# Performance work log

Hardware: AMD Instinct MI355X
Metric: run time of the kernel (lower is better)

The kernel has to match this reference:

```python
import jax, jax.numpy as jnp
import numpy as np

N, K, CIN, COUT, HF, WF = 8, 8, 128, 128, 64, 64
HT, WT = 128, 128
WIN_H = 20


def cos_window(size, h):
    t = np.linspace(0.0, np.pi / 2, h)
    s = np.sin(t)
    win = np.ones(size, dtype=np.float64)
    win[:h, :] = s[:, None]
    win[-h:, :] = s[::-1][:, None]
    win[:, :h] = s[None, :]
    win[:, -h:] = s[::-1][None, :]
    t2 = np.pi / 2 - np.sqrt(t[:, None] ** 2 + t[None, :] ** 2)
    s2 = np.sin(np.clip(t2, 0.0, None))
    win[:h, :h] = s2[::-1, ::-1]
    win[:h, -h:] = s2[::-1, :]
    win[-h:, :h] = s2[:, ::-1]
    win[-h:, -h:] = s2
    return win.astype(np.float32)


def setup_inputs() -> dict:
    key = jax.random.key(0)
    k1, k2, k3, k4 = jax.random.split(key, 4)
    x = jax.random.normal(k1, (N * K, CIN, HF, WF), dtype=jnp.float32)
    conv_w = jax.random.normal(k2, (COUT, CIN), dtype=jnp.float32) / np.sqrt(CIN).astype(np.float32)
    conv_b = jax.random.normal(k3, (COUT,), dtype=jnp.float32) * 0.1
    qs = jax.random.uniform(k4, (N, K, 2), dtype=jnp.float32, minval=0.5, maxval=1.5)
    rng = np.random.default_rng(0)
    bx = rng.integers(-8, 48, (N, K))
    by = rng.integers(-8, 48, (N, K))
    bw = rng.integers(32, 112, (N, K))
    bh = rng.integers(32, 112, (N, K))
    boxes = jnp.asarray(np.stack([bx, by, bx + bw, by + bh], axis=-1).astype(np.int32))
    win = jnp.asarray(cos_window((HT, WT), WIN_H))
    return {"x": x, "conv_w": conv_w, "conv_b": conv_b, "win": win, "qs": qs, "boxes": boxes}


def _sample(img, u, v):
    # img [C,H,W]; separable bilinear gather at row coords u [HT], col coords v [WT]
    # (equivalent to F.interpolate(..., align_corners=True) resize + paste at box offset)
    C, H, W = img.shape
    u0 = jnp.clip(jnp.floor(u), 0, H - 2).astype(jnp.int32)
    du = jnp.clip(u - u0, 0.0, 1.0)
    rows = img[:, u0, :] * (1.0 - du)[None, :, None] + img[:, u0 + 1, :] * du[None, :, None]
    v0 = jnp.clip(jnp.floor(v), 0, W - 2).astype(jnp.int32)
    dv = jnp.clip(v - v0, 0.0, 1.0)
    return rows[:, :, v0] * (1.0 - dv)[None, None, :] + rows[:, :, v0 + 1] * dv[None, None, :]


def _splat(crop, box, win, q1, use_win):
    # One crop -> weighted contribution on the full [HT,WT] canvas (masked to its box).
    Hc, Wc = crop.shape[-2:]
    Hw, Ww = win.shape
    x, y, x1, y1 = box[0], box[1], box[2], box[3]
    h = (y1 - y).astype(jnp.float32)
    w = (x1 - x).astype(jnp.float32)
    Ys = jnp.arange(HT, dtype=jnp.float32)
    Xs = jnp.arange(WT, dtype=jnp.float32)
    dy = Ys - y
    dx = Xs - x
    u = dy * (Hc - 1) / jnp.maximum(h - 1.0, 1.0)
    v = dx * (Wc - 1) / jnp.maximum(w - 1.0, 1.0)
    uw = dy * (Hw - 1) / jnp.maximum(h - 1.0, 1.0)
    vw = dx * (Ww - 1) / jnp.maximum(w - 1.0, 1.0)
    mask = ((dy >= 0) & (Ys < y1))[:, None] & ((dx >= 0) & (Xs < x1))[None, :]
    sampled = _sample(crop, u, v)                    # [C,HT,WT]
    wwin = _sample(win[None], uw, vw)[0]             # [HT,WT]
    weight = jnp.where(use_win, wwin, 1.0) * mask    # first crop skips the window
    return sampled * (weight * q1)[None], weight


def _average(crops, boxes_b, q1_b, win):
    # crops [K,C,HF,WF]; overlapping weighted accumulation into shared canvas
    use_win = jnp.arange(crops.shape[0]) > 0
    ci, cw = jax.vmap(_splat, in_axes=(0, 0, None, 0, 0))(crops, boxes_b, win, q1_b, use_win)
    a_img = ci.sum(0)
    a_w = cw.sum(0)
    return a_img / jnp.maximum(a_w, 1e-6)[None]


def reference(x, conv_w, conv_b, win, qs, boxes):
    # layer: 1x1 conv
    f = jnp.einsum('bchw,oc->bohw', x, conv_w) + conv_b[None, :, None, None]
    fr = f.reshape(N, K, COUT, HF, WF)
    # qi = 1/q[:,1]; crops accumulated as resized*weight*q[:,1]
    fa = jax.vmap(_average, in_axes=(0, 0, 0, None))(fr, boxes, qs[:, :, 1], win)
    return fa  # forward_mode == 1
```

## Files before the change

### kernel.cpp

```cpp
#include <hip/hip_runtime.h>
#include <hip/hip_fp16.h>

#define NN 8
#define KK 8
#define CI 128
#define CO 128
#define HT 128
#define WT 128

typedef __attribute__((ext_vector_type(8))) _Float16 f16x8;
typedef __attribute__((ext_vector_type(4))) float f32x4;

__device__ __forceinline__ unsigned short f2h_bits(float v) {
    _Float16 h = (_Float16)v;
    unsigned short b;
    __builtin_memcpy(&b, &h, 2);
    return b;
}
__device__ __forceinline__ float hLO(unsigned int u) {
    unsigned short b = (unsigned short)(u & 0xffffu);
    _Float16 h; __builtin_memcpy(&h, &b, 2);
    return (float)h;
}
__device__ __forceinline__ float hHI(unsigned int u) {
    unsigned short b = (unsigned short)(u >> 16);
    _Float16 h; __builtin_memcpy(&h, &b, 2);
    return (float)h;
}

__global__ __launch_bounds__(256) void k_conv(const float* __restrict__ x,
                                              const float* __restrict__ Wm,
                                              const float* __restrict__ bias,
                                              unsigned short* __restrict__ f) {
    __shared__ unsigned char lds[65536];
    int t = threadIdx.x;
    int b = blockIdx.y;
    int px0 = blockIdx.x * 128;
    const float* xb = x + (size_t)b * CI * 4096;

    #pragma unroll
    for (int p = 0; p < 8; ++p) {
        int px = (t & 63) + 64 * (p & 1);
        int c0 = 8 * ((t >> 6) + 4 * (p >> 1));
        unsigned int v0w, v1w, v2w, v3w;
        {
            unsigned short s0 = f2h_bits(xb[(size_t)(c0 + 0) * 4096 + px0 + px]);
            unsigned short s1 = f2h_bits(xb[(size_t)(c0 + 1) * 4096 + px0 + px]);
            unsigned short s2 = f2h_bits(xb[(size_t)(c0 + 2) * 4096 + px0 + px]);
            unsigned short s3 = f2h_bits(xb[(size_t)(c0 + 3) * 4096 + px0 + px]);
            unsigned short s4 = f2h_bits(xb[(size_t)(c0 + 4) * 4096 + px0 + px]);
            unsigned short s5 = f2h_bits(xb[(size_t)(c0 + 5) * 4096 + px0 + px]);
            unsigned short s6 = f2h_bits(xb[(size_t)(c0 + 6) * 4096 + px0 + px]);
            unsigned short s7 = f2h_bits(xb[(size_t)(c0 + 7) * 4096 + px0 + px]);
            v0w = (unsigned int)s0 | ((unsigned int)s1 << 16);
            v1w = (unsigned int)s2 | ((unsigned int)s3 << 16);
            v2w = (unsigned int)s4 | ((unsigned int)s5 << 16);
            v3w = (unsigned int)s6 | ((unsigned int)s7 << 16);
        }
        int L = px * 256 + c0 * 2;
        L ^= ((px & 15) << 4);
        uint4 pk; pk.x = v0w; pk.y = v1w; pk.z = v2w; pk.w = v3w;
        *(uint4*)(lds + L) = pk;
    }
    #pragma unroll
    for (int p = 0; p < 16; ++p) {
        int o = (t >> 5) + 8 * p;
        int c0 = (t & 31) * 4;
        float4 wv = *(const float4*)(Wm + o * CI + c0);
        unsigned int w0 = (unsigned int)f2h_bits(wv.x) | ((unsigned int)f2h_bits(wv.y) << 16);
        unsigned int w1 = (unsigned int)f2h_bits(wv.z) | ((unsigned int)f2h_bits(wv.w) << 16);
        int L = 32768 + o * 256 + c0 * 2;
        L ^= ((o & 15) << 4);
        uint2 pk; pk.x = w0; pk.y = w1;
        *(uint2*)(lds + L) = pk;
    }
    __syncthreads();

    int wid = t >> 6;
    int l   = t & 63;
    int lr  = l & 15;
    int lk  = l >> 4;

    f32x4 acc[2][8];
    #pragma unroll
    for (int m = 0; m < 2; ++m)
        #pragma unroll
        for (int j = 0; j < 8; ++j)
            acc[m][j] = (f32x4){0.f, 0.f, 0.f, 0.f};

    #pragma unroll
    for (int s = 0; s < 4; ++s) {
        int c = s * 32 + lk * 8;
        f16x8 afr[2], bfr[8];
        #pragma unroll
        for (int m = 0; m < 2; ++m) {
            int px = wid * 32 + m * 16 + lr;
            int L = px * 256 + c * 2;
            L ^= ((px & 15) << 4);
            afr[m] = *(const f16x8*)(lds + L);
        }
        #pragma unroll
        for (int j = 0; j < 8; ++j) {
            int o = j * 16 + lr;
            int L = 32768 + o * 256 + c * 2;
            L ^= ((o & 15) << 4);
            bfr[j] = *(const f16x8*)(lds + L);
        }
        #pragma unroll
        for (int m = 0; m < 2; ++m)
            #pragma unroll
            for (int j = 0; j < 8; ++j)
                acc[m][j] = __builtin_amdgcn_mfma_f32_16x16x32_f16(afr[m], bfr[j], acc[m][j], 0, 0, 0);
    }

    float bs[8];
    #pragma unroll
    for (int j = 0; j < 8; ++j) bs[j] = bias[j * 16 + lr];
    #pragma unroll
    for (int m = 0; m < 2; ++m) {
        int pxb = px0 + wid * 32 + m * 16 + lk * 4;
        #pragma unroll
        for (int j = 0; j < 8; ++j) {
            int o = j * 16 + lr;
            #pragma unroll
            for (int r = 0; r < 4; ++r) {
                float v = acc[m][j][r] + bs[j];
                f[((size_t)b * 4096 + (pxb + r)) * CO + o] = f2h_bits(v);
            }
        }
    }
}

__global__ __launch_bounds__(256) void k_sample(const unsigned short* __restrict__ f,
                                                const float* __restrict__ win,
                                                const float* __restrict__ qs,
                                                const int* __restrict__ boxes,
                                                float* __restrict__ out) {
    int t = threadIdx.x;
    int n = blockIdx.y;
    int Yi = blockIdx.x;
    int X = t & 127;
    int og = t >> 7;

    float acc[64];
    #pragma unroll
    for (int i = 0; i < 64; ++i) acc[i] = 0.f;
    float wsum = 0.f;

    for (int k = 0; k < KK; ++k) {
        const int* bp = boxes + (n * KK + k) * 4;
        int bx = bp[0], by = bp[1], bx1 = bp[2], by1 = bp[3];
        int hh = by1 - by, ww = bx1 - bx;
        int dyi = Yi - by, dxi = X - bx;
        bool mask = (dyi >= 0) && (Yi < by1) && (dxi >= 0) && (X < bx1);

        float dy = (float)dyi, dx = (float)dxi;
        float denY = fmaxf((float)hh - 1.f, 1.f);
        float denX = fmaxf((float)ww - 1.f, 1.f);
        float invY = 1.0f / denY;
        float invX = 1.0f / denX;
        float fy = dy * invY;
        float fx = dx * invX;

        float weight = 0.f;
        if (mask) {
            if (k == 0) {
                weight = 1.f;
            } else {
                float uw = fy * 127.0f;
                float vw = fx * 127.0f;
                int u0w = min(max((int)floorf(uw), 0), 126);
                int v0w = min(max((int)floorf(vw), 0), 126);
                float duw = fminf(fmaxf(uw - (float)u0w, 0.f), 1.f);
                float dvw = fminf(fmaxf(vw - (float)v0w, 0.f), 1.f);
                const float* wp = win + u0w * WT + v0w;
                float a = wp[0], b2 = wp[1], c2 = wp[WT], d2 = wp[WT + 1];
                float r_v0 = a  * (1.f - duw) + c2 * duw;
                float r_v1 = b2 * (1.f - duw) + d2 * duw;
                weight = r_v0 * (1.f - dvw) + r_v1 * dvw;
            }
        }
        wsum += weight;
        float q1 = qs[(n * KK + k) * 2 + 1];
        float wk = weight * q1;

        if (wk != 0.f) {
            float u = fy * 63.0f;
            float v = fx * 63.0f;
            int u0 = min(max((int)floorf(u), 0), 62);
            int v0 = min(max((int)floorf(v), 0), 62);
            float du = fminf(fmaxf(u - (float)u0, 0.f), 1.f);
            float dv = fminf(fmaxf(v - (float)v0, 0.f), 1.f);
            float w11 = du * dv * wk;
            float w10 = du * (1.f - dv) * wk;
            float w01 = (1.f - du) * dv * wk;
            float w00 = (1.f - du) * (1.f - dv) * wk;
            const unsigned short* pA =
                f + ((size_t)((n * KK + k) * 4096 + u0 * 64 + v0)) * CO + og * 64;
            #pragma unroll
            for (int ch = 0; ch < 8; ++ch) {
                uint4 A = *(const uint4*)(pA + ch * 8);
                uint4 B = *(const uint4*)(pA + CO + ch * 8);
                uint4 C = *(const uint4*)(pA + 64 * CO + ch * 8);
                uint4 D = *(const uint4*)(pA + 65 * CO + ch * 8);
#define DO_PAIR(ae, be, ce, de, o0)                                             \
                acc[o0]     += w00 * hLO(ae) + w01 * hLO(be)                    \
                             + w10 * hLO(ce) + w11 * hLO(de);                   \
                acc[(o0)+1] += w00 * hHI(ae) + w01 * hHI(be)                    \
                             + w10 * hHI(ce) + w11 * hHI(de);
                DO_PAIR(A.x, B.x, C.x, D.x, ch * 8 + 0)
                DO_PAIR(A.y, B.y, C.y, D.y, ch * 8 + 2)
                DO_PAIR(A.z, B.z, C.z, D.z, ch * 8 + 4)
                DO_PAIR(A.w, B.w, C.w, D.w, ch * 8 + 6)
#undef DO_PAIR
            }
        }
    }

    float den = fmaxf(wsum, 1e-6f);
    float id = 1.f / den;
    #pragma unroll
    for (int i = 0; i < 64; ++i) {
        int o = og * 64 + i;
        out[((size_t)n * CO + o) * 16384 + Yi * 128 + X] = acc[i] * id;
    }
}

extern "C" void kernel_launch(void* const* d_in, const int* in_sizes, int n_in,
                              void* d_out, int out_size, void* d_ws, size_t ws_size,
                              hipStream_t stream) {
    const float* x    = (const float*)d_in[0];
    const float* Wm   = (const float*)d_in[1];
    const float* bias = (const float*)d_in[2];
    const float* win  = (const float*)d_in[3];
    const float* qs   = (const float*)d_in[4];
    const int*   bxs  = (const int*)d_in[5];
    float* out = (float*)d_out;

    unsigned short* f = (unsigned short*)d_ws;

    hipLaunchKernelGGL(k_conv,   dim3(32, 64), dim3(256), 0, stream, x, Wm, bias, f);
    hipLaunchKernelGGL(k_sample, dim3(128, 8), dim3(256), 0, stream, f, win, qs, bxs, out);
}
```

Baseline: 108.0 us.

## Precast conv weights to fp16 once and split sample channels over more threads

A new single-block prep kernel converts the conv weights to fp16 in workspace. The conv kernel then reads B fragments straight from global/L2 instead of staging them in LDS, which halves its LDS footprint so more blocks can be resident. The sampling kernel now uses 512 threads per block, each owning 32 output channels instead of 64, to cut accumulator register pressure and raise parallelism. In exchange it adds an extra launch and uncached-in-LDS weight loads inside the MFMA loop.

```diff
diff --git a/kernel.cpp b/kernel.cpp
--- a/kernel.cpp
+++ b/kernel.cpp
@@ -28,11 +28,25 @@
     return (float)h;
 }
 
+__global__ __launch_bounds__(256) void k_prep(const float* __restrict__ Wm,
+                                              unsigned short* __restrict__ Wh) {
+    int t = threadIdx.x;
+    #pragma unroll
+    for (int i = 0; i < 16; ++i) {
+        int idx4 = t + i * 256;
+        float4 wv = *(const float4*)(Wm + idx4 * 4);
+        uint2 pk;
+        pk.x = (unsigned int)f2h_bits(wv.x) | ((unsigned int)f2h_bits(wv.y) << 16);
+        pk.y = (unsigned int)f2h_bits(wv.z) | ((unsigned int)f2h_bits(wv.w) << 16);
+        *(uint2*)(Wh + idx4 * 4) = pk;
+    }
+}
+
 __global__ __launch_bounds__(256) void k_conv(const float* __restrict__ x,
-                                              const float* __restrict__ Wm,
+                                              const unsigned short* __restrict__ Wh,
                                               const float* __restrict__ bias,
                                               unsigned short* __restrict__ f) {
-    __shared__ unsigned char lds[65536];
+    __shared__ unsigned char lds[32768];
     int t = threadIdx.x;
     int b = blockIdx.y;
     int px0 = blockIdx.x * 128;
@@ -62,18 +76,6 @@
         uint4 pk; pk.x = v0w; pk.y = v1w; pk.z = v2w; pk.w = v3w;
         *(uint4*)(lds + L) = pk;
     }
-    #pragma unroll
-    for (int p = 0; p < 16; ++p) {
-        int o = (t >> 5) + 8 * p;
-        int c0 = (t & 31) * 4;
-        float4 wv = *(const float4*)(Wm + o * CI + c0);
-        unsigned int w0 = (unsigned int)f2h_bits(wv.x) | ((unsigned int)f2h_bits(wv.y) << 16);
-        unsigned int w1 = (unsigned int)f2h_bits(wv.z) | ((unsigned int)f2h_bits(wv.w) << 16);
-        int L = 32768 + o * 256 + c0 * 2;
-        L ^= ((o & 15) << 4);
-        uint2 pk; pk.x = w0; pk.y = w1;
-        *(uint2*)(lds + L) = pk;
-    }
     __syncthreads();
 
     int wid = t >> 6;
@@ -102,9 +104,7 @@
         #pragma unroll
         for (int j = 0; j < 8; ++j) {
             int o = j * 16 + lr;
-            int L = 32768 + o * 256 + c * 2;
-            L ^= ((o & 15) << 4);
-            bfr[j] = *(const f16x8*)(lds + L);
+            bfr[j] = *(const f16x8*)(Wh + o * CI + c);
         }
         #pragma unroll
         for (int m = 0; m < 2; ++m)
@@ -131,7 +131,7 @@
     }
 }
 
-__global__ __launch_bounds__(256) void k_sample(const unsigned short* __restrict__ f,
+__global__ __launch_bounds__(512) void k_sample(const unsigned short* __restrict__ f,
                                                 const float* __restrict__ win,
                                                 const float* __restrict__ qs,
                                                 const int* __restrict__ boxes,
@@ -142,9 +142,9 @@
     int X = t & 127;
     int og = t >> 7;
 
-    float acc[64];
-    #pragma unroll
-    for (int i = 0; i < 64; ++i) acc[i] = 0.f;
+    float acc[32];
+    #pragma unroll
+    for (int i = 0; i < 32; ++i) acc[i] = 0.f;
     float wsum = 0.f;
 
     for (int k = 0; k < KK; ++k) {
@@ -196,9 +196,9 @@
             float w01 = (1.f - du) * dv * wk;
             float w00 = (1.f - du) * (1.f - dv) * wk;
             const unsigned short* pA =
-                f + ((size_t)((n * KK + k) * 4096 + u0 * 64 + v0)) * CO + og * 64;
+                f + ((size_t)((n * KK + k) * 4096 + u0 * 64 + v0)) * CO + og * 32;
             #pragma unroll
-            for (int ch = 0; ch < 8; ++ch) {
+            for (int ch = 0; ch < 4; ++ch) {
                 uint4 A = *(const uint4*)(pA + ch * 8);
                 uint4 B = *(const uint4*)(pA + CO + ch * 8);
                 uint4 C = *(const uint4*)(pA + 64 * CO + ch * 8);
@@ -220,8 +220,8 @@
     float den = fmaxf(wsum, 1e-6f);
     float id = 1.f / den;
     #pragma unroll
-    for (int i = 0; i < 64; ++i) {
-        int o = og * 64 + i;
+    for (int i = 0; i < 32; ++i) {
+        int o = og * 32 + i;
         out[((size_t)n * CO + o) * 16384 + Yi * 128 + X] = acc[i] * id;
     }
 }
@@ -237,8 +237,11 @@
     const int*   bxs  = (const int*)d_in[5];
     float* out = (float*)d_out;
 
-    unsigned short* f = (unsigned short*)d_ws;
-
-    hipLaunchKernelGGL(k_conv,   dim3(32, 64), dim3(256), 0, stream, x, Wm, bias, f);
-    hipLaunchKernelGGL(k_sample, dim3(128, 8), dim3(256), 0, stream, f, win, qs, bxs, out);
-}
+    unsigned char* ws = (unsigned char*)d_ws;
+    unsigned short* f  = (unsigned short*)ws;
+    unsigned short* Wh = (unsigned short*)(ws + 67108864);
+
+    hipLaunchKernelGGL(k_prep,  dim3(1),        dim3(256), 0, stream, Wm, Wh);
+    hipLaunchKernelGGL(k_conv,  dim3(32, 64),   dim3(256), 0, stream, x, Wh, bias, f);
+    hipLaunchKernelGGL(k_sample, dim3(128, 8),  dim3(512), 0, stream, f, win, qs, bxs, out);
+}
```

Measured after the change: 133.0 us. 1.23x slower.
